# Performance work log

Hardware: AMD Instinct MI355X
Metric: run time of the kernel (lower is better)

The kernel has to match this reference:

```python
import jax, jax.numpy as jnp
import numpy as np

T, WS, SHIFT, HEADS, DIM = 5, (8, 8), (4, 4), 6, 192
HEAD_DIM = DIM // HEADS
SCALE = HEAD_DIM ** -0.5
MLP_HID = 4 * DIM
TABLE_LEN = (T * 2 * WS[0] - 1) * (2 * WS[1] - 1)


def _rel_index():
    # exact replica of WindowAttention.__init__ index construction (t,h,w coords)
    ct, ch, cw = np.arange(T), np.arange(WS[0]), np.arange(WS[1])
    coords = np.stack(np.meshgrid(ct, ch, cw, indexing='ij')).reshape(3, -1)
    rel = (coords[:, :, None] - coords[:, None, :]).transpose(1, 2, 0).astype(np.int64)
    rel[:, :, 0] += WS[0] - 1
    rel[:, :, 1] += WS[1] - 1
    rel[:, :, 0] *= 2 * WS[1] - 1
    return jnp.asarray(rel.sum(-1))  # (N, N)


def _attn_mask(H, W):
    # standard shifted-window mask on (H,W); identical across T, so tile (T,T)
    img = np.zeros((H, W), np.float32)
    cnt = 0
    for hs in (slice(0, -WS[0]), slice(-WS[0], -SHIFT[0]), slice(-SHIFT[0], None)):
        for ws_ in (slice(0, -WS[1]), slice(-WS[1], -SHIFT[1]), slice(-SHIFT[1], None)):
            img[hs, ws_] = cnt
            cnt += 1
    img = img.reshape(H // WS[0], WS[0], W // WS[1], WS[1]).transpose(0, 2, 1, 3)
    img = img.reshape(-1, WS[0] * WS[1])  # (nW, Wh*Ww)
    m = img[:, None, :] - img[:, :, None]
    m = np.where(m != 0, -100.0, 0.0).astype(np.float32)
    return jnp.asarray(np.tile(m, (1, T, T)))  # (nW, T*Wh*Ww, T*Wh*Ww)


def _win_part(x, ws):
    B, t, H, W, C = x.shape
    x = x.reshape(B, t, H // ws[0], ws[0], W // ws[1], ws[1], C)
    return x.transpose(0, 2, 4, 1, 3, 5, 6).reshape(-1, t * ws[0] * ws[1], C)


def _win_rev(w, ws, H, W, t, B):
    x = w.reshape(B, H // ws[0], W // ws[1], t, ws[0], ws[1], -1)
    return x.transpose(0, 3, 1, 4, 2, 5, 6).reshape(B, t, H, W, -1)


def _ln(x, g, b):
    mu = x.mean(-1, keepdims=True)
    var = ((x - mu) ** 2).mean(-1, keepdims=True)
    return (x - mu) * jax.lax.rsqrt(var + 1e-5) * g + b


def _forward(x, ln1_g, ln1_b, qkv_w, qkv_b, rel_bias_table, proj_w, proj_b,
             ln2_g, ln2_b, fc1_w, fc1_b, fc2_w, fc2_b, H, W):
    B, L, C = x.shape
    shortcut = x
    h = _ln(x, ln1_g, ln1_b)
    qkv = h @ qkv_w.T + qkv_b                                   # (B, L, 3C)
    qkv = qkv.reshape(B, T, H, W, 3 * C)
    qkv = jnp.roll(qkv, (-SHIFT[0], -SHIFT[1]), axis=(2, 3))
    qkv = _win_part(qkv, WS)                                    # (B_, N, 3C)
    B_, N, _ = qkv.shape
    qkv = qkv.reshape(B_, N, 3, HEADS, HEAD_DIM).transpose(2, 0, 3, 1, 4)
    q, k, v = qkv[0], qkv[1], qkv[2]
    attn = jnp.einsum('bhnd,bhmd->bhnm', q * SCALE, k)          # (B_, H, N, N)
    bias = rel_bias_table[_rel_index()].transpose(2, 0, 1)      # (heads, N, N)
    attn = attn + bias[None]
    mask = _attn_mask(H, W)                                     # (nW, N, N)
    nW = mask.shape[0]
    attn = attn.reshape(B_ // nW, nW, HEADS, N, N) + mask[None, :, None]
    attn = jax.nn.softmax(attn.reshape(B_, HEADS, N, N), axis=-1)
    out = jnp.einsum('bhnm,bhmd->bhnd', attn, v)
    out = out.transpose(0, 2, 1, 3).reshape(B_, N, C)
    out = out @ proj_w.T + proj_b
    out = _win_rev(out, WS, H, W, T, B)
    out = jnp.roll(out, (SHIFT[0], SHIFT[1]), axis=(2, 3)).reshape(B, L, C)
    x = shortcut + out
    h = _ln(x, ln2_g, ln2_b)
    h = jax.nn.gelu(h @ fc1_w.T + fc1_b, approximate=False) @ fc2_w.T + fc2_b
    return x + h


def setup_inputs() -> dict:
    key = jax.random.key(0)
    ks = jax.random.split(key, 8)
    B, Himg, Wimg = 2, 64, 64
    L = T * Himg * Wimg
    s = 0.02
    return {
        'x': jax.random.normal(ks[0], (B, L, DIM), jnp.float32),
        'ln1_g': jnp.ones((DIM,), jnp.float32),
        'ln1_b': jnp.zeros((DIM,), jnp.float32),
        'qkv_w': jax.random.normal(ks[1], (3 * DIM, DIM), jnp.float32) * s,
        'qkv_b': jnp.zeros((3 * DIM,), jnp.float32),
        'rel_bias_table': jax.random.normal(ks[2], (TABLE_LEN, HEADS), jnp.float32) * s,
        'proj_w': jax.random.normal(ks[3], (DIM, DIM), jnp.float32) * s,
        'proj_b': jnp.zeros((DIM,), jnp.float32),
        'ln2_g': jnp.ones((DIM,), jnp.float32),
        'ln2_b': jnp.zeros((DIM,), jnp.float32),
        'fc1_w': jax.random.normal(ks[4], (MLP_HID, DIM), jnp.float32) * s,
        'fc1_b': jnp.zeros((MLP_HID,), jnp.float32),
        'fc2_w': jax.random.normal(ks[5], (DIM, MLP_HID), jnp.float32) * s,
        'fc2_b': jnp.zeros((DIM,), jnp.float32),
        'H': Himg,
        'W': Wimg,
    }


def reference(x, ln1_g, ln1_b, qkv_w, qkv_b, rel_bias_table, proj_w, proj_b,
              ln2_g, ln2_b, fc1_w, fc1_b, fc2_w, fc2_b, H, W):
    return _forward(x, ln1_g, ln1_b, qkv_w, qkv_b, rel_bias_table, proj_w, proj_b,
                    ln2_g, ln2_b, fc1_w, fc1_b, fc2_w, fc2_b, H, W)
```

## Files before the change

kernel.cpp:

```cpp
#include <hip/hip_runtime.h>
#include <math.h>

typedef unsigned short u16;
typedef unsigned int u32;
typedef short bf16x8 __attribute__((ext_vector_type(8)));
typedef float f32x4 __attribute__((ext_vector_type(4)));
typedef _Float16 f16x4 __attribute__((ext_vector_type(4)));

#define TT 5
#define HEADS 6
#define HD 32
#define DIM 192
#define NWIN 320
#define LTOK (TT*64*64)
#define BATCH 2
#define MROWS (BATCH*LTOK)
#define QSCALE 0.17677669529663687f
#define LOG2E 1.4426950408889634f
#define QSCALE2 (QSCALE * LOG2E)
#define MASK2 (-100.0f * LOG2E)

__device__ __forceinline__ u16 f2bf(float f) {
    u32 u = __float_as_uint(f);
    u32 r = (u + 0x7FFFu + ((u >> 16) & 1u)) >> 16;
    return (u16)r;
}
__device__ __forceinline__ float bflo(u32 u) { return __uint_as_float(u << 16); }
__device__ __forceinline__ float bfhi(u32 u) { return __uint_as_float(u & 0xFFFF0000u); }
__device__ __forceinline__ u32 pkh(float a, float b) {
    auto h = __builtin_amdgcn_cvt_pkrtz(a, b);
    return __builtin_bit_cast(u32, h);
}
#if __has_builtin(__builtin_amdgcn_exp2f)
__device__ __forceinline__ float ex2(float x) { return __builtin_amdgcn_exp2f(x); }
#else
__device__ __forceinline__ float ex2(float x) {
    float r; asm("v_exp_f32 %0, %1" : "=v"(r) : "v"(x)); return r;
}
#endif

__global__ __launch_bounds__(256) void cvt4_kernel(
    const float* __restrict__ a, const float* __restrict__ b,
    const float* __restrict__ c, const float* __restrict__ d,
    u16* __restrict__ oa, u16* __restrict__ ob,
    u16* __restrict__ oc, u16* __restrict__ od)
{
    int i = blockIdx.x * 256 + threadIdx.x;
    if (i < 110592)       oa[i]          = f2bf(a[i]);
    else if (i < 147456)  ob[i - 110592] = f2bf(b[i - 110592]);
    else if (i < 294912)  oc[i - 147456] = f2bf(c[i - 147456]);
    else                  od[i - 294912] = f2bf(d[i - 294912]);
}

__global__ __launch_bounds__(256) void ln_kernel(
    const float* __restrict__ x, const float* __restrict__ g,
    const float* __restrict__ b, u16* __restrict__ out)
{
    int tok  = blockIdx.x * 4 + (threadIdx.x >> 6);
    int lane = threadIdx.x & 63;
    const float* xr = x + (size_t)tok * DIM;
    float v0 = xr[lane], v1 = xr[lane + 64], v2 = xr[lane + 128];
    float s = v0 + v1 + v2;
    #pragma unroll
    for (int off = 32; off; off >>= 1) s += __shfl_xor(s, off, 64);
    float mu = s * (1.0f / 192.0f);
    float d0 = v0 - mu, d1 = v1 - mu, d2 = v2 - mu;
    float vs = d0 * d0 + d1 * d1 + d2 * d2;
    #pragma unroll
    for (int off = 32; off; off >>= 1) vs += __shfl_xor(vs, off, 64);
    float rstd = rsqrtf(vs * (1.0f / 192.0f) + 1e-5f);
    u16* orow = out + (size_t)tok * DIM;
    orow[lane]       = f2bf(d0 * rstd * g[lane]       + b[lane]);
    orow[lane + 64]  = f2bf(d1 * rstd * g[lane + 64]  + b[lane + 64]);
    orow[lane + 128] = f2bf(d2 * rstd * g[lane + 128] + b[lane + 128]);
}

template<int EPI>
__global__ __launch_bounds__(256) void mfma_gemm(
    const u16* __restrict__ A, const u16* __restrict__ W,
    const float* __restrict__ bias, void* __restrict__ outp,
    const float* __restrict__ xin, int N, int K)
{
    __shared__ u16 As[128 * 64];
    __shared__ u16 Bs[64 * 64];
    const int tid  = threadIdx.x;
    const int lane = tid & 63, wv = tid >> 6;
    const int ln16 = lane & 15, quad = lane >> 4;

    const int flat  = blockIdx.y * gridDim.x + blockIdx.x;
    const int cpx   = (gridDim.x * gridDim.y) >> 3;
    const int nf    = (flat & 7) * cpx + (flat >> 3);
    const int bn    = nf % gridDim.x;
    const int bm    = nf / gridDim.x;

    const int srow = lane >> 3;
    const int sxor = (lane & 7) ^ srow;
    const int acol = sxor * 8;

    f32x4 acc[2][4] = {};

    for (int k0 = 0; k0 < K; k0 += 64) {
        __syncthreads();
        #pragma unroll
        for (int a = 0; a < 4; ++a) {
            const u16* g = A + (size_t)(bm * 128 + a * 32 + wv * 8 + srow) * K + k0 + acol;
            __builtin_amdgcn_global_load_lds(
                (const __attribute__((address_space(1))) u32*)g,
                (__attribute__((address_space(3))) u32*)((char*)As + a * 4096 + wv * 1024),
                16, 0, 0);
        }
        #pragma unroll
        for (int bb = 0; bb < 2; ++bb) {
            const u16* g = W + (size_t)(bn * 64 + bb * 32 + wv * 8 + srow) * K + k0 + acol;
            __builtin_amdgcn_global_load_lds(
                (const __attribute__((address_space(1))) u32*)g,
                (__attribute__((address_space(3))) u32*)((char*)Bs + bb * 4096 + wv * 1024),
                16, 0, 0);
        }
        __syncthreads();
        #pragma unroll
        for (int s = 0; s < 2; ++s) {
            bf16x8 af[2], bf[4];
            #pragma unroll
            for (int i = 0; i < 2; ++i) {
                int r = wv * 32 + i * 16 + ln16;
                int slot = (s * 4 + quad) ^ (r & 7);
                af[i] = *(const bf16x8*)((const char*)As + r * 128 + slot * 16);
            }
            #pragma unroll
            for (int j = 0; j < 4; ++j) {
                int r = j * 16 + ln16;
                int slot = (s * 4 + quad) ^ (r & 7);
                bf[j] = *(const bf16x8*)((const char*)Bs + r * 128 + slot * 16);
            }
            #pragma unroll
            for (int i = 0; i < 2; ++i)
                #pragma unroll
                for (int j = 0; j < 4; ++j)
                    acc[i][j] = __builtin_amdgcn_mfma_f32_16x16x32_bf16(
                        af[i], bf[j], acc[i][j], 0, 0, 0);
        }
    }

    #pragma unroll
    for (int i = 0; i < 2; ++i) {
        int gr0 = bm * 128 + wv * 32 + i * 16 + quad * 4;
        #pragma unroll
        for (int j = 0; j < 4; ++j) {
            int gc = bn * 64 + j * 16 + ln16;
            float bv = bias[gc];
            #pragma unroll
            for (int rr = 0; rr < 4; ++rr) {
                int gr = gr0 + rr;
                float val = acc[i][j][rr] + bv;
                if (EPI == 0) {
                    ((u16*)outp)[(size_t)gr * N + gc] = f2bf(val);
                } else if (EPI == 1) {
                    float gl = val * 0.5f * (1.0f + erff(val * 0.70710678118654752f));
                    ((u16*)outp)[(size_t)gr * N + gc] = f2bf(gl);
                } else if (EPI == 2) {
                    size_t dst = (size_t)gr * N + gc;
                    ((float*)outp)[dst] = xin[dst] + val;
                } else {
                    ((float*)outp)[(size_t)gr * N + gc] += val;
                }
            }
        }
    }
}

__global__ __launch_bounds__(320) void attn_kernel(
    const u16* __restrict__ qkv, const float* __restrict__ table,
    u16* __restrict__ attout)
{
    const int head = blockIdx.x % HEADS;
    const int b_   = blockIdx.x / HEADS;
    const int b = b_ >> 6, hb = (b_ >> 3) & 7, wb = b_ & 7;
    const int tid = threadIdx.x;
    const int lane = tid & 63, wv = tid >> 6;
    const int ln16 = lane & 15, quad = lane >> 4;

    __shared__ u16 Ks[320 * 40];
    __shared__ u16 Vt[32 * 328];
    __shared__ u16 meta[320];
    __shared__ float tbl[188];

    {
        int n = tid;
        int t1 = n >> 6, r1 = (n >> 3) & 7, c1 = n & 7;
        int h1 = hb * 8 + r1, w1 = wb * 8 + c1;
        int l1 = t1 * 4096 + ((h1 + 4) & 63) * 64 + ((w1 + 4) & 63);
        const u16* src = qkv + ((size_t)b * LTOK + l1) * (3 * DIM) + head * HD;
        const uint4* k4 = (const uint4*)(src + DIM);
        #pragma unroll
        for (int i = 0; i < 4; ++i)
            *(uint4*)(Ks + n * 40 + i * 8) = k4[i];
        const uint4* v4 = (const uint4*)(src + 2 * DIM);
        #pragma unroll
        for (int i = 0; i < 4; ++i) {
            uint4 u = v4[i];
            u32 ws[4] = {u.x, u.y, u.z, u.w};
            #pragma unroll
            for (int j = 0; j < 4; ++j) {
                u32 hb2 = pkh(bflo(ws[j]), bfhi(ws[j]));
                int d = i * 8 + j * 2;
                Vt[d * 328 + n]       = (u16)(hb2 & 0xFFFF);
                Vt[(d + 1) * 328 + n] = (u16)(hb2 >> 16);
            }
        }
        int off = (7 - t1) * 15 + 7 - r1 - c1;
        int rh = h1 < 56 ? 0 : (h1 < 60 ? 1 : 2);
        int rw = w1 < 56 ? 0 : (w1 < 60 ? 1 : 2);
        meta[n] = (u16)(off | ((rh * 3 + rw) << 8));
        if (n < 187) tbl[n] = table[n * HEADS + head] * LOG2E;
    }

    bf16x8 qf[4];
    int basen[4], myreg[4];
    #pragma unroll
    for (int qt = 0; qt < 4; ++qt) {
        int nq = wv * 64 + qt * 16 + ln16;
        int t1 = nq >> 6, r1 = (nq >> 3) & 7, c1 = nq & 7;
        int h1 = hb * 8 + r1, w1 = wb * 8 + c1;
        int l1 = t1 * 4096 + ((h1 + 4) & 63) * 64 + ((w1 + 4) & 63);
        qf[qt] = *(const bf16x8*)(qkv + ((size_t)b * LTOK + l1) * (3 * DIM)
                                  + head * HD + quad * 8);
        basen[qt] = t1 * 15 + r1 + c1;
        int rh = h1 < 56 ? 0 : (h1 < 60 ? 1 : 2);
        int rw = w1 < 56 ? 0 : (w1 < 60 ? 1 : 2);
        myreg[qt] = rh * 3 + rw;
    }

    __syncthreads();

    f32x4 o[4][2] = {};
    float l_[4] = {};
    const f32x4 zero = {};

    #pragma unroll 1
    for (int c = 0; c < 10; ++c) {
        int kb = c * 32;
        bf16x8 af0 = *(const bf16x8*)(Ks + (kb + ln16) * 40 + quad * 8);
        bf16x8 af1 = *(const bf16x8*)(Ks + (kb + 16 + ln16) * 40 + quad * 8);
        f16x4 va[2][2];
        #pragma unroll
        for (int dt = 0; dt < 2; ++dt)
            #pragma unroll
            for (int kt = 0; kt < 2; ++kt)
                va[dt][kt] = *(const f16x4*)(Vt + (dt * 16 + ln16) * 328
                                             + kb + kt * 16 + quad * 4);
        ushort4 m4a = *(const ushort4*)(meta + kb + quad * 4);
        ushort4 m4b = *(const ushort4*)(meta + kb + 16 + quad * 4);
        u16 mta[4] = {m4a.x, m4a.y, m4a.z, m4a.w};
        u16 mtb[4] = {m4b.x, m4b.y, m4b.z, m4b.w};

        #pragma unroll
        for (int qt = 0; qt < 4; ++qt) {
            f32x4 s0 = __builtin_amdgcn_mfma_f32_16x16x32_bf16(af0, qf[qt], zero, 0, 0, 0);
            f32x4 s1 = __builtin_amdgcn_mfma_f32_16x16x32_bf16(af1, qf[qt], zero, 0, 0, 0);
            float p[8];
            #pragma unroll
            for (int r = 0; r < 4; ++r) {
                int ma = mta[r], mb = mtb[r];
                float va0 = fmaf(s0[r], QSCALE2, tbl[basen[qt] + (ma & 0xFF)]);
                float vb0 = fmaf(s1[r], QSCALE2, tbl[basen[qt] + (mb & 0xFF)]);
                p[r]     = va0 + (((ma >> 8) == myreg[qt]) ? 0.0f : MASK2);
                p[4 + r] = vb0 + (((mb >> 8) == myreg[qt]) ? 0.0f : MASK2);
            }
            float ls = 0.0f;
            #pragma unroll
            for (int j = 0; j < 8; ++j) { p[j] = ex2(p[j]); ls += p[j]; }
            l_[qt] += ls;
            uint2 pk0 = { pkh(p[0], p[1]), pkh(p[2], p[3]) };
            uint2 pk1 = { pkh(p[4], p[5]), pkh(p[6], p[7]) };
            f16x4 pf0 = __builtin_bit_cast(f16x4, pk0);
            f16x4 pf1 = __builtin_bit_cast(f16x4, pk1);
            #pragma unroll
            for (int dt = 0; dt < 2; ++dt) {
                o[qt][dt] = __builtin_amdgcn_mfma_f32_16x16x16f16(va[dt][0], pf0, o[qt][dt], 0, 0, 0);
                o[qt][dt] = __builtin_amdgcn_mfma_f32_16x16x16f16(va[dt][1], pf1, o[qt][dt], 0, 0, 0);
            }
        }
    }

    #pragma unroll
    for (int qt = 0; qt < 4; ++qt) {
        float lt = l_[qt];
        lt += __shfl_xor(lt, 16, 64);
        lt += __shfl_xor(lt, 32, 64);
        float inv = 1.0f / lt;
        int nq = wv * 64 + qt * 16 + ln16;
        int t1 = nq >> 6, r1 = (nq >> 3) & 7, c1 = nq & 7;
        int h1 = hb * 8 + r1, w1 = wb * 8 + c1;
        int l1 = t1 * 4096 + ((h1 + 4) & 63) * 64 + ((w1 + 4) & 63);
        u16* dst = attout + ((size_t)b * LTOK + l1) * DIM + head * HD + quad * 4;
        #pragma unroll
        for (int dt = 0; dt < 2; ++dt) {
            u32 w0 = (u32)f2bf(o[qt][dt][0] * inv) | ((u32)f2bf(o[qt][dt][1] * inv) << 16);
            u32 w1 = (u32)f2bf(o[qt][dt][2] * inv) | ((u32)f2bf(o[qt][dt][3] * inv) << 16);
            uint2 st = {w0, w1};
            *(uint2*)(dst + dt * 16) = st;
        }
    }
}

extern "C" void kernel_launch(void* const* d_in, const int* in_sizes, int n_in,
                              void* d_out, int out_size, void* d_ws, size_t ws_size,
                              hipStream_t stream)
{
    (void)in_sizes; (void)n_in; (void)out_size; (void)ws_size;
    const float* x      = (const float*)d_in[0];
    const float* ln1_g  = (const float*)d_in[1];
    const float* ln1_b  = (const float*)d_in[2];
    const float* qkv_w  = (const float*)d_in[3];
    const float* qkv_b  = (const float*)d_in[4];
    const float* table  = (const float*)d_in[5];
    const float* proj_w = (const float*)d_in[6];
    const float* proj_b = (const float*)d_in[7];
    const float* ln2_g  = (const float*)d_in[8];
    const float* ln2_b  = (const float*)d_in[9];
    const float* fc1_w  = (const float*)d_in[10];
    const float* fc1_b  = (const float*)d_in[11];
    const float* fc2_w  = (const float*)d_in[12];
    const float* fc2_b  = (const float*)d_in[13];
    float* out = (float*)d_out;

    u16* wsu     = (u16*)d_ws;
    u16* h_buf   = wsu;
    u16* qkv_buf = wsu + (size_t)MROWS * DIM;
    u16* att_buf = wsu + (size_t)MROWS * (4 * DIM);
    u16* fc1_buf = wsu + (size_t)MROWS * DIM;
    u16* wq = wsu + (size_t)MROWS * (5 * DIM);
    u16* wp = wq + 3 * DIM * DIM;
    u16* w1 = wp + DIM * DIM;
    u16* w2 = w1 + 4 * DIM * DIM;

    cvt4_kernel<<<(12 * DIM * DIM) / 256, 256, 0, stream>>>(
        qkv_w, proj_w, fc1_w, fc2_w, wq, wp, w1, w2);

    ln_kernel<<<MROWS / 4, 256, 0, stream>>>(x, ln1_g, ln1_b, h_buf);
    mfma_gemm<0><<<dim3(3 * DIM / 64, MROWS / 128), 256, 0, stream>>>(
        h_buf, wq, qkv_b, qkv_buf, nullptr, 3 * DIM, DIM);
    attn_kernel<<<128 * HEADS, 320, 0, stream>>>(qkv_buf, table, att_buf);
    mfma_gemm<2><<<dim3(DIM / 64, MROWS / 128), 256, 0, stream>>>(
        att_buf, wp, proj_b, out, x, DIM, DIM);
    ln_kernel<<<MROWS / 4, 256, 0, stream>>>(out, ln2_g, ln2_b, h_buf);
    mfma_gemm<1><<<dim3(4 * DIM / 64, MROWS / 128), 256, 0, stream>>>(
        h_buf, w1, fc1_b, fc1_buf, nullptr, 4 * DIM, DIM);
    mfma_gemm<3><<<dim3(DIM / 64, MROWS / 128), 256, 0, stream>>>(
        fc1_buf, w2, fc2_b, out, nullptr, DIM, 4 * DIM);
}
```

Measured before the change: 259.0 us.

## Specialize K=192 GEMMs: stage full weight tile in LDS, read A directly

Makes K a template parameter. For K=192 the GEMM loads the whole 64x192 weight tile into LDS once with a single barrier, and feeds the A operand straight from global memory into registers instead of through LDS. This removes the per-k-step barriers and the A staging for the QKV, proj and fc1 GEMMs. The cost is uncoalesced-ish direct global A reads (each lane reads 16 bytes from separate rows) and more LDS per block.

Result: slower. 265.1 us (+2.4%).

```diff
diff --git a/kernel.cpp b/kernel.cpp
--- a/kernel.cpp
+++ b/kernel.cpp
@@ -75,14 +75,12 @@
     orow[lane + 128] = f2bf(d2 * rstd * g[lane + 128] + b[lane + 128]);
 }
 
-template<int EPI>
+template<int EPI, int KK>
 __global__ __launch_bounds__(256) void mfma_gemm(
     const u16* __restrict__ A, const u16* __restrict__ W,
     const float* __restrict__ bias, void* __restrict__ outp,
-    const float* __restrict__ xin, int N, int K)
-{
-    __shared__ u16 As[128 * 64];
-    __shared__ u16 Bs[64 * 64];
+    const float* __restrict__ xin, int N)
+{
     const int tid  = threadIdx.x;
     const int lane = tid & 63, wv = tid >> 6;
     const int ln16 = lane & 15, quad = lane >> 4;
@@ -99,46 +97,86 @@
 
     f32x4 acc[2][4] = {};
 
-    for (int k0 = 0; k0 < K; k0 += 64) {
-        __syncthreads();
-        #pragma unroll
-        for (int a = 0; a < 4; ++a) {
-            const u16* g = A + (size_t)(bm * 128 + a * 32 + wv * 8 + srow) * K + k0 + acol;
+    if constexpr (KK == 192) {
+        __shared__ u16 Bs[12288];
+        #pragma unroll
+        for (int bb = 0; bb < 6; ++bb) {
+            const u16* g = W + (size_t)(bn * 64 + (bb & 1) * 32 + wv * 8 + srow) * KK
+                           + (bb >> 1) * 64 + acol;
             __builtin_amdgcn_global_load_lds(
                 (const __attribute__((address_space(1))) u32*)g,
-                (__attribute__((address_space(3))) u32*)((char*)As + a * 4096 + wv * 1024),
+                (__attribute__((address_space(3))) u32*)
+                    ((char*)Bs + (bb >> 1) * 8192 + (bb & 1) * 4096 + wv * 1024),
                 16, 0, 0);
         }
-        #pragma unroll
-        for (int bb = 0; bb < 2; ++bb) {
-            const u16* g = W + (size_t)(bn * 64 + bb * 32 + wv * 8 + srow) * K + k0 + acol;
-            __builtin_amdgcn_global_load_lds(
-                (const __attribute__((address_space(1))) u32*)g,
-                (__attribute__((address_space(3))) u32*)((char*)Bs + bb * 4096 + wv * 1024),
-                16, 0, 0);
-        }
+        const u16* abase = A + (size_t)(bm * 128 + wv * 32 + ln16) * KK + quad * 8;
         __syncthreads();
         #pragma unroll
-        for (int s = 0; s < 2; ++s) {
-            bf16x8 af[2], bf[4];
-            #pragma unroll
-            for (int i = 0; i < 2; ++i) {
-                int r = wv * 32 + i * 16 + ln16;
-                int slot = (s * 4 + quad) ^ (r & 7);
-                af[i] = *(const bf16x8*)((const char*)As + r * 128 + slot * 16);
-            }
-            #pragma unroll
-            for (int j = 0; j < 4; ++j) {
-                int r = j * 16 + ln16;
-                int slot = (s * 4 + quad) ^ (r & 7);
-                bf[j] = *(const bf16x8*)((const char*)Bs + r * 128 + slot * 16);
-            }
-            #pragma unroll
-            for (int i = 0; i < 2; ++i)
-                #pragma unroll
-                for (int j = 0; j < 4; ++j)
-                    acc[i][j] = __builtin_amdgcn_mfma_f32_16x16x32_bf16(
-                        af[i], bf[j], acc[i][j], 0, 0, 0);
+        for (int c = 0; c < 3; ++c) {
+            #pragma unroll
+            for (int s = 0; s < 2; ++s) {
+                bf16x8 af[2], bf[4];
+                #pragma unroll
+                for (int i = 0; i < 2; ++i)
+                    af[i] = *(const bf16x8*)(abase + (size_t)i * 16 * KK + c * 64 + s * 32);
+                #pragma unroll
+                for (int j = 0; j < 4; ++j) {
+                    int r = j * 16 + ln16;
+                    int slot = (s * 4 + quad) ^ (r & 7);
+                    bf[j] = *(const bf16x8*)((const char*)Bs + c * 8192 + r * 128 + slot * 16);
+                }
+                #pragma unroll
+                for (int i = 0; i < 2; ++i)
+                    #pragma unroll
+                    for (int j = 0; j < 4; ++j)
+                        acc[i][j] = __builtin_amdgcn_mfma_f32_16x16x32_bf16(
+                            af[i], bf[j], acc[i][j], 0, 0, 0);
+            }
+        }
+    } else {
+        __shared__ u16 As[128 * 64];
+        __shared__ u16 Bs[64 * 64];
+        for (int k0 = 0; k0 < KK; k0 += 64) {
+            __syncthreads();
+            #pragma unroll
+            for (int a = 0; a < 4; ++a) {
+                const u16* g = A + (size_t)(bm * 128 + a * 32 + wv * 8 + srow) * KK + k0 + acol;
+                __builtin_amdgcn_global_load_lds(
+                    (const __attribute__((address_space(1))) u32*)g,
+                    (__attribute__((address_space(3))) u32*)((char*)As + a * 4096 + wv * 1024),
+                    16, 0, 0);
+            }
+            #pragma unroll
+            for (int bb = 0; bb < 2; ++bb) {
+                const u16* g = W + (size_t)(bn * 64 + bb * 32 + wv * 8 + srow) * KK + k0 + acol;
+                __builtin_amdgcn_global_load_lds(
+                    (const __attribute__((address_space(1))) u32*)g,
+                    (__attribute__((address_space(3))) u32*)((char*)Bs + bb * 4096 + wv * 1024),
+                    16, 0, 0);
+            }
+            __syncthreads();
+            #pragma unroll
+            for (int s = 0; s < 2; ++s) {
+                bf16x8 af[2], bf[4];
+                #pragma unroll
+                for (int i = 0; i < 2; ++i) {
+                    int r = wv * 32 + i * 16 + ln16;
+                    int slot = (s * 4 + quad) ^ (r & 7);
+                    af[i] = *(const bf16x8*)((const char*)As + r * 128 + slot * 16);
+                }
+                #pragma unroll
+                for (int j = 0; j < 4; ++j) {
+                    int r = j * 16 + ln16;
+                    int slot = (s * 4 + quad) ^ (r & 7);
+                    bf[j] = *(const bf16x8*)((const char*)Bs + r * 128 + slot * 16);
+                }
+                #pragma unroll
+                for (int i = 0; i < 2; ++i)
+                    #pragma unroll
+                    for (int j = 0; j < 4; ++j)
+                        acc[i][j] = __builtin_amdgcn_mfma_f32_16x16x32_bf16(
+                            af[i], bf[j], acc[i][j], 0, 0, 0);
+            }
         }
     }
 
@@ -339,14 +377,14 @@
         qkv_w, proj_w, fc1_w, fc2_w, wq, wp, w1, w2);
 
     ln_kernel<<<MROWS / 4, 256, 0, stream>>>(x, ln1_g, ln1_b, h_buf);
-    mfma_gemm<0><<<dim3(3 * DIM / 64, MROWS / 128), 256, 0, stream>>>(
-        h_buf, wq, qkv_b, qkv_buf, nullptr, 3 * DIM, DIM);
+    mfma_gemm<0, 192><<<dim3(3 * DIM / 64, MROWS / 128), 256, 0, stream>>>(
+        h_buf, wq, qkv_b, qkv_buf, nullptr, 3 * DIM);
     attn_kernel<<<128 * HEADS, 320, 0, stream>>>(qkv_buf, table, att_buf);
-    mfma_gemm<2><<<dim3(DIM / 64, MROWS / 128), 256, 0, stream>>>(
-        att_buf, wp, proj_b, out, x, DIM, DIM);
+    mfma_gemm<2, 192><<<dim3(DIM / 64, MROWS / 128), 256, 0, stream>>>(
+        att_buf, wp, proj_b, out, x, DIM);
     ln_kernel<<<MROWS / 4, 256, 0, stream>>>(out, ln2_g, ln2_b, h_buf);
-    mfma_gemm<1><<<dim3(4 * DIM / 64, MROWS / 128), 256, 0, stream>>>(
-        h_buf, w1, fc1_b, fc1_buf, nullptr, 4 * DIM, DIM);
-    mfma_gemm<3><<<dim3(DIM / 64, MROWS / 128), 256, 0, stream>>>(
-        fc1_buf, w2, fc2_b, out, nullptr, DIM, 4 * DIM);
-}
+    mfma_gemm<1, 192><<<dim3(4 * DIM / 64, MROWS / 128), 256, 0, stream>>>(
+        h_buf, w1, fc1_b, fc1_buf, nullptr, 4 * DIM);
+    mfma_gemm<3, 768><<<dim3(DIM / 64, MROWS / 128), 256, 0, stream>>>(
+        fc1_buf, w2, fc2_b, out, nullptr, DIM);
+}
```
